# Optimization experiments

Measured on AMD Instinct MI355X. Metric: run time of the kernel, lower is better.

Reference implementation:

```python
import jax, jax.numpy as jnp
import numpy as np
import itertools

B, T, D, H, E, K = 2, 1024, 768, 3072, 8, 2


def _trigram_dirs():
    # 8 vertices of the cube {-1,+1}^3, L2-normalized rows (matches F.normalize)
    t = np.array(list(itertools.product([-1.0, 1.0], repeat=3)), dtype=np.float32)[:E]
    t = t / np.linalg.norm(t, axis=1, keepdims=True)
    return jnp.asarray(t)


def setup_inputs() -> dict:
    key = jax.random.key(0)
    k1, k2, k3, k4 = jax.random.split(key, 4)
    x = jax.random.normal(k1, (B, T, D), jnp.float32)
    Wr = jax.random.normal(k2, (3, D), jnp.float32) * 0.02
    W1 = jax.random.normal(k3, (E, D, H), jnp.float32) * 0.02
    W2 = jax.random.normal(k4, (E, H, D), jnp.float32) * 0.02
    return {"x": x, "Wr": Wr, "W1": W1, "W2": W2}


def reference(x, Wr, W1, W2):
    Bb, Tt, Dd = x.shape
    xf = x.reshape(-1, Dd)                       # (N, D)
    dirs = _trigram_dirs()                       # (E, 3)
    z3 = xf @ Wr.T                               # (N, 3)
    logits = z3 @ dirs.T                         # (N, E)
    probs = jax.nn.softmax(logits, axis=-1)
    topv, topi = jax.lax.top_k(probs, K)         # (N, K)
    topv = topv / topv.sum(axis=-1, keepdims=True)
    N = xf.shape[0]
    # dense gate matrix: gates[n, e] = sum_k topv[n,k] * [topi[n,k]==e]
    gates = jnp.zeros((N, E), xf.dtype).at[jnp.arange(N)[:, None], topi].add(topv)
    # dense-all-experts equivalent of the masked gather/scatter loop
    h = jax.nn.gelu(jnp.einsum('nd,edh->neh', xf, W1), approximate=False)
    y = jnp.einsum('neh,ehd->ned', h, W2)
    out = jnp.einsum('ne,ned->nd', gates, y).reshape(Bb, Tt, Dd)
    tokens_per_expert = probs.mean(axis=0)
    aux_loss = 0.01 * jnp.mean((tokens_per_expert - 1.0 / E) ** 2)
    return out, aux_loss
```

## Files before the change

kernel.cpp:

```cpp
#include <hip/hip_runtime.h>
#include <hip/hip_bf16.h>
#include <math.h>

#define DD 768
#define HH 3072
#define EE 8
#define NN 2048
#define PP 5120
#define PT 40

typedef __attribute__((ext_vector_type(8))) short short8;
typedef __attribute__((ext_vector_type(4))) float floatx4;

typedef const __attribute__((address_space(1))) void gas_void;
typedef __attribute__((address_space(3))) void las_void;

__device__ __forceinline__ void gld16(const void* g, void* l) {
    __builtin_amdgcn_global_load_lds((gas_void*)g, (las_void*)l, 16, 0, 0);
}

__device__ __forceinline__ unsigned short f2bf(float f) {
    union { float f; unsigned int u; } v; v.f = f;
    unsigned int u = v.u;
    u += 0x7fffu + ((u >> 16) & 1u);
    return (unsigned short)(u >> 16);
}

__global__ __launch_bounds__(256) void routing_kernel(
    const float* __restrict__ x, const float* __restrict__ Wr,
    int* __restrict__ counts, float* __restrict__ psum,
    int* __restrict__ top_e, float* __restrict__ top_g)
{
    __shared__ float wr[3 * DD];
    __shared__ float lpsum[EE];
    int tid = threadIdx.x;
    for (int i = tid; i < 3 * DD; i += 256) wr[i] = Wr[i];
    if (tid < EE) lpsum[tid] = 0.f;
    __syncthreads();

    int n = blockIdx.x * 256 + tid;
    const float4* xp = (const float4*)(x + (size_t)n * DD);
    float z0 = 0.f, z1 = 0.f, z2 = 0.f;
#pragma unroll 8
    for (int i = 0; i < DD / 4; i++) {
        float4 v = xp[i];
        int d = i * 4;
        z0 = fmaf(v.x, wr[d], z0);         z0 = fmaf(v.y, wr[d+1], z0);
        z0 = fmaf(v.z, wr[d+2], z0);       z0 = fmaf(v.w, wr[d+3], z0);
        z1 = fmaf(v.x, wr[DD+d], z1);      z1 = fmaf(v.y, wr[DD+d+1], z1);
        z1 = fmaf(v.z, wr[DD+d+2], z1);    z1 = fmaf(v.w, wr[DD+d+3], z1);
        z2 = fmaf(v.x, wr[2*DD+d], z2);    z2 = fmaf(v.y, wr[2*DD+d+1], z2);
        z2 = fmaf(v.z, wr[2*DD+d+2], z2);  z2 = fmaf(v.w, wr[2*DD+d+3], z2);
    }

    const float r3 = 0.57735026918962576f;
    float p[EE];
    float mx = -1e30f;
#pragma unroll
    for (int e = 0; e < EE; e++) {
        float s0 = (e & 4) ? z0 : -z0;
        float s1 = (e & 2) ? z1 : -z1;
        float s2 = (e & 1) ? z2 : -z2;
        p[e] = (s0 + s1 + s2) * r3;
        mx = fmaxf(mx, p[e]);
    }
    float sum = 0.f;
#pragma unroll
    for (int e = 0; e < EE; e++) { p[e] = expf(p[e] - mx); sum += p[e]; }
    float inv_s = 1.f / sum;
#pragma unroll
    for (int e = 0; e < EE; e++) p[e] *= inv_s;

    int e1 = 0; float p1 = p[0];
#pragma unroll
    for (int e = 1; e < EE; e++) if (p[e] > p1) { p1 = p[e]; e1 = e; }
    int e2 = -1; float p2 = -1.f;
#pragma unroll
    for (int e = 0; e < EE; e++) if (e != e1 && p[e] > p2) { p2 = p[e]; e2 = e; }
    float inv_t = 1.f / (p1 + p2);
    top_e[2*n]   = e1;  top_g[2*n]   = p1 * inv_t;
    top_e[2*n+1] = e2;  top_g[2*n+1] = p2 * inv_t;
    atomicAdd(&counts[e1], 1);
    atomicAdd(&counts[e2], 1);

#pragma unroll
    for (int e = 0; e < EE; e++) atomicAdd(&lpsum[e], p[e]);
    __syncthreads();
    if (tid < EE) atomicAdd(&psum[tid], lpsum[tid]);
}

__global__ void scan_aux_kernel(const int* __restrict__ counts, const float* __restrict__ psum,
                                int* __restrict__ cursor, int* __restrict__ poffs,
                                float* __restrict__ out_aux)
{
    if (threadIdx.x == 0) {
        int run = 0;
        for (int e = 0; e < EE; e++) {
            poffs[e] = run;
            cursor[e] = run;
            run += ((counts[e] + 127) >> 7) << 7;
        }
        poffs[EE] = run;
        float s = 0.f;
        for (int e = 0; e < EE; e++) {
            float t = psum[e] * (1.f / NN) - (1.f / EE);
            s += t * t;
        }
        *out_aux = 0.01f * (s * (1.f / EE));
    }
}

__global__ __launch_bounds__(256) void scatter_kernel(
    const int* __restrict__ top_e, int* __restrict__ cursor,
    int* __restrict__ row_tok, int* __restrict__ inv_row)
{
    int n = blockIdx.x * 256 + threadIdx.x;
#pragma unroll
    for (int k = 0; k < 2; k++) {
        int e = top_e[2*n + k];
        int pos = atomicAdd(&cursor[e], 1);
        row_tok[pos]    = n;
        inv_row[2*n+k]  = pos;
    }
}

__global__ __launch_bounds__(192) void gather_cast_kernel(
    const float* __restrict__ x, const int* __restrict__ counts,
    const int* __restrict__ poffs, const int* __restrict__ row_tok,
    unsigned short* __restrict__ xg)
{
    int t = threadIdx.x;
    int pr = blockIdx.x * 4 + t / 48;
    int c0 = (t % 48) * 16;
    int e = 0;
#pragma unroll
    for (int i = 0; i < EE - 1; i++) if (pr >= poffs[i + 1]) e = i + 1;
    int local = pr - poffs[e];
    unsigned short* dst = xg + (size_t)pr * DD + c0;
    if (local < counts[e]) {
        int tok = row_tok[pr];
        const float4* sp = (const float4*)(x + (size_t)tok * DD + c0);
        alignas(16) unsigned short tmp[16];
#pragma unroll
        for (int j = 0; j < 4; j++) {
            float4 v = sp[j];
            tmp[4*j+0] = f2bf(v.x); tmp[4*j+1] = f2bf(v.y);
            tmp[4*j+2] = f2bf(v.z); tmp[4*j+3] = f2bf(v.w);
        }
        *(uint4*)dst       = *(uint4*)&tmp[0];
        *(uint4*)(dst + 8) = *(uint4*)&tmp[8];
    } else {
        uint4 z = {0, 0, 0, 0};
        *(uint4*)dst       = z;
        *(uint4*)(dst + 8) = z;
    }
}

__global__ __launch_bounds__(256) void transpose_cast_kernel(
    const float* __restrict__ W1, const float* __restrict__ W2,
    unsigned short* __restrict__ w1t, unsigned short* __restrict__ w2t)
{
    int z = blockIdx.z, e = blockIdx.y, bx = blockIdx.x;
    const float* src; unsigned short* dst; int R, C, rt, ct;
    if (z == 0) { R = DD; C = HH; src = W1 + (size_t)e * R * C; dst = w1t + (size_t)e * R * C; }
    else        { R = HH; C = DD; src = W2 + (size_t)e * R * C; dst = w2t + (size_t)e * R * C; }
    rt = bx / (C / 64); ct = bx % (C / 64);
    int r0 = rt * 64, c0 = ct * 64;

    __shared__ unsigned short tile[64][66];
    int tid = threadIdx.x;
    int lr = tid >> 2, lc = (tid & 3) * 16;
    const float4* sp = (const float4*)(src + (size_t)(r0 + lr) * C + c0 + lc);
#pragma unroll
    for (int j = 0; j < 4; j++) {
        float4 v = sp[j];
        tile[lr][lc + 4*j + 0] = f2bf(v.x);
        tile[lr][lc + 4*j + 1] = f2bf(v.y);
        tile[lr][lc + 4*j + 2] = f2bf(v.z);
        tile[lr][lc + 4*j + 3] = f2bf(v.w);
    }
    __syncthreads();
    int oc = tid >> 2, orr = (tid & 3) * 16;
    alignas(16) unsigned short tmp[16];
#pragma unroll
    for (int j = 0; j < 16; j++) tmp[j] = tile[orr + j][oc];
    unsigned short* dp = dst + (size_t)(c0 + oc) * R + r0 + orr;
    *(uint4*)dp       = *(uint4*)&tmp[0];
    *(uint4*)(dp + 8) = *(uint4*)&tmp[8];
}

__global__ __launch_bounds__(256) void gemm1_kernel(
    const unsigned short* __restrict__ xg, const unsigned short* __restrict__ w1t,
    unsigned short* __restrict__ h, const int* __restrict__ poffs)
{
    int t = blockIdx.x;
    if (t * 128 >= poffs[EE]) return;
    int e = 0;
#pragma unroll
    for (int i = 0; i < EE - 1; i++) if (t * 128 >= poffs[i + 1]) e = i + 1;
    int row0 = t * 128, n0 = blockIdx.y * 128;

    __shared__ alignas(16) unsigned short As[2][128][32];
    __shared__ alignas(16) unsigned short Bs[2][128][32];

    int tid = threadIdx.x;
    int w = tid >> 6, lane = tid & 63;
    int quad = lane >> 4, l15 = lane & 15;
    int wm = (w & 1) * 64, wn = (w >> 1) * 64;

    const unsigned short* abase = xg + (size_t)row0 * DD;
    const unsigned short* bbase = w1t + (size_t)e * HH * DD + (size_t)n0 * DD;

    int c0 = w * 64 + lane, c1 = 256 + c0;
    const unsigned short* ga0 = abase + (c0 >> 2) * DD + (c0 & 3) * 8;
    const unsigned short* ga1 = abase + (c1 >> 2) * DD + (c1 & 3) * 8;
    const unsigned short* gb0 = bbase + (c0 >> 2) * DD + (c0 & 3) * 8;
    const unsigned short* gb1 = bbase + (c1 >> 2) * DD + (c1 & 3) * 8;
    int lofs0 = (w * 64) * 8;
    int lofs1 = (256 + w * 64) * 8;

    floatx4 acc[4][4];
#pragma unroll
    for (int i = 0; i < 4; i++)
#pragma unroll
        for (int j = 0; j < 4; j++)
#pragma unroll
            for (int r = 0; r < 4; r++) acc[i][j][r] = 0.f;

    const int NT = DD / 32;
    gld16(ga0, &As[0][0][0] + lofs0);
    gld16(ga1, &As[0][0][0] + lofs1);
    gld16(gb0, &Bs[0][0][0] + lofs0);
    gld16(gb1, &Bs[0][0][0] + lofs1);
    __syncthreads();

    for (int kt = 0; kt < NT; kt++) {
        int cur = kt & 1;
        if (kt + 1 < NT) {
            int k0 = (kt + 1) * 32;
            unsigned short* nA = &As[cur ^ 1][0][0];
            unsigned short* nB = &Bs[cur ^ 1][0][0];
            gld16(ga0 + k0, nA + lofs0);
            gld16(ga1 + k0, nA + lofs1);
            gld16(gb0 + k0, nB + lofs0);
            gld16(gb1 + k0, nB + lofs1);
        }
        short8 afr[4], bfr[4];
#pragma unroll
        for (int fm = 0; fm < 4; fm++) afr[fm] = *(const short8*)&As[cur][wm + fm*16 + l15][quad * 8];
#pragma unroll
        for (int fn = 0; fn < 4; fn++) bfr[fn] = *(const short8*)&Bs[cur][wn + fn*16 + l15][quad * 8];
#pragma unroll
        for (int fm = 0; fm < 4; fm++)
#pragma unroll
            for (int fn = 0; fn < 4; fn++)
                acc[fm][fn] = __builtin_amdgcn_mfma_f32_16x16x32_bf16(afr[fm], bfr[fn], acc[fm][fn], 0, 0, 0);
        __syncthreads();
    }

#pragma unroll
    for (int fm = 0; fm < 4; fm++)
#pragma unroll
        for (int r = 0; r < 4; r++) {
            int rt = wm + fm * 16 + quad * 4 + r;
            size_t hrow = (size_t)(row0 + rt) * HH;
#pragma unroll
            for (int fn = 0; fn < 4; fn++) {
                int col = n0 + wn + fn * 16 + l15;
                float v = acc[fm][fn][r];
                float g = 0.5f * v * (1.f + erff(v * 0.70710678118654752f));
                h[hrow + col] = f2bf(g);
            }
        }
}

__global__ __launch_bounds__(256) void gemm2_kernel(
    const unsigned short* __restrict__ h, const unsigned short* __restrict__ w2t,
    float* __restrict__ ybuf, const int* __restrict__ poffs)
{
    int t = blockIdx.x;
    if (t * 128 >= poffs[EE]) return;
    int e = 0;
#pragma unroll
    for (int i = 0; i < EE - 1; i++) if (t * 128 >= poffs[i + 1]) e = i + 1;
    int row0 = t * 128, n0 = blockIdx.y * 128;
    int kz = blockIdx.z;

    __shared__ alignas(16) unsigned short As[2][128][32];
    __shared__ alignas(16) unsigned short Bs[2][128][32];

    int tid = threadIdx.x;
    int w = tid >> 6, lane = tid & 63;
    int quad = lane >> 4, l15 = lane & 15;
    int wm = (w & 1) * 64, wn = (w >> 1) * 64;

    const unsigned short* abase = h + (size_t)row0 * HH + kz * (HH / 2);
    const unsigned short* bbase = w2t + (size_t)e * DD * HH + (size_t)n0 * HH + kz * (HH / 2);

    int c0 = w * 64 + lane, c1 = 256 + c0;
    const unsigned short* ga0 = abase + (c0 >> 2) * HH + (c0 & 3) * 8;
    const unsigned short* ga1 = abase + (c1 >> 2) * HH + (c1 & 3) * 8;
    const unsigned short* gb0 = bbase + (c0 >> 2) * HH + (c0 & 3) * 8;
    const unsigned short* gb1 = bbase + (c1 >> 2) * HH + (c1 & 3) * 8;
    int lofs0 = (w * 64) * 8;
    int lofs1 = (256 + w * 64) * 8;

    floatx4 acc[4][4];
#pragma unroll
    for (int i = 0; i < 4; i++)
#pragma unroll
        for (int j = 0; j < 4; j++)
#pragma unroll
            for (int r = 0; r < 4; r++) acc[i][j][r] = 0.f;

    const int NT = (HH / 2) / 32;
    gld16(ga0, &As[0][0][0] + lofs0);
    gld16(ga1, &As[0][0][0] + lofs1);
    gld16(gb0, &Bs[0][0][0] + lofs0);
    gld16(gb1, &Bs[0][0][0] + lofs1);
    __syncthreads();

    for (int kt = 0; kt < NT; kt++) {
        int cur = kt & 1;
        if (kt + 1 < NT) {
            int k0 = (kt + 1) * 32;
            unsigned short* nA = &As[cur ^ 1][0][0];
            unsigned short* nB = &Bs[cur ^ 1][0][0];
            gld16(ga0 + k0, nA + lofs0);
            gld16(ga1 + k0, nA + lofs1);
            gld16(gb0 + k0, nB + lofs0);
            gld16(gb1 + k0, nB + lofs1);
        }
        short8 afr[4], bfr[4];
#pragma unroll
        for (int fm = 0; fm < 4; fm++) afr[fm] = *(const short8*)&As[cur][wm + fm*16 + l15][quad * 8];
#pragma unroll
        for (int fn = 0; fn < 4; fn++) bfr[fn] = *(const short8*)&Bs[cur][wn + fn*16 + l15][quad * 8];
#pragma unroll
        for (int fm = 0; fm < 4; fm++)
#pragma unroll
            for (int fn = 0; fn < 4; fn++)
                acc[fm][fn] = __builtin_amdgcn_mfma_f32_16x16x32_bf16(afr[fm], bfr[fn], acc[fm][fn], 0, 0, 0);
        __syncthreads();
    }

    float* yb = ybuf + (size_t)kz * PP * DD + (size_t)row0 * DD;
#pragma unroll
    for (int fm = 0; fm < 4; fm++)
#pragma unroll
        for (int r = 0; r < 4; r++) {
            int rt = wm + fm * 16 + quad * 4 + r;
            float* op = yb + (size_t)rt * DD + n0 + wn;
#pragma unroll
            for (int fn = 0; fn < 4; fn++)
                op[fn * 16 + l15] = acc[fm][fn][r];
        }
}

__global__ __launch_bounds__(192) void combine_kernel(
    const float* __restrict__ ybuf, const int* __restrict__ inv_row,
    const float* __restrict__ top_g, float* __restrict__ out)
{
    int n = blockIdx.x;
    int c = threadIdx.x * 4;
    int r0 = inv_row[2*n], r1 = inv_row[2*n+1];
    float g0 = top_g[2*n], g1 = top_g[2*n+1];
    const size_t S = (size_t)PP * DD;
    const float* y0 = ybuf + (size_t)r0 * DD + c;
    const float* y1 = ybuf + (size_t)r1 * DD + c;
    float4 a0 = *(const float4*)y0, b0 = *(const float4*)(y0 + S);
    float4 a1 = *(const float4*)y1, b1 = *(const float4*)(y1 + S);
    float4 o;
    o.x = g0 * (a0.x + b0.x) + g1 * (a1.x + b1.x);
    o.y = g0 * (a0.y + b0.y) + g1 * (a1.y + b1.y);
    o.z = g0 * (a0.z + b0.z) + g1 * (a1.z + b1.z);
    o.w = g0 * (a0.w + b0.w) + g1 * (a1.w + b1.w);
    *(float4*)(out + (size_t)n * DD + c) = o;
}

extern "C" void kernel_launch(void* const* d_in, const int* in_sizes, int n_in,
                              void* d_out, int out_size, void* d_ws, size_t ws_size,
                              hipStream_t stream)
{
    const float* x  = (const float*)d_in[0];
    const float* Wr = (const float*)d_in[1];
    const float* W1 = (const float*)d_in[2];
    const float* W2 = (const float*)d_in[3];
    float* out = (float*)d_out;

    char* ws = (char*)d_ws;
    int*   counts   = (int*)(ws + 0);
    int*   cursor   = (int*)(ws + 32);
    float* psum     = (float*)(ws + 64);
    int*   poffs    = (int*)(ws + 96);
    int*   top_e    = (int*)(ws + 1024);
    float* top_g    = (float*)(ws + 1024 + 16384);
    int*   row_tok  = (int*)(ws + 1024 + 2 * 16384);
    int*   inv_row  = (int*)(ws + 1024 + 2 * 16384 + PP * 4);
    size_t off = (size_t)(1024 + 2 * 16384 + PP * 4 + 16384 + 255) & ~(size_t)255;
    unsigned short* xg  = (unsigned short*)(ws + off); off += (size_t)PP * DD * 2;
    unsigned short* hbf = (unsigned short*)(ws + off); off += (size_t)PP * HH * 2;
    unsigned short* w1t = (unsigned short*)(ws + off); off += (size_t)EE * DD * HH * 2;
    unsigned short* w2t = (unsigned short*)(ws + off);
    float* ybuf = (float*)w1t;

    hipMemsetAsync(ws, 0, 96, stream);

    transpose_cast_kernel<<<dim3(576, EE, 2), 256, 0, stream>>>(W1, W2, w1t, w2t);
    routing_kernel<<<dim3(NN / 256), 256, 0, stream>>>(x, Wr, counts, psum, top_e, top_g);
    scan_aux_kernel<<<1, 64, 0, stream>>>(counts, psum, cursor, poffs, out + (size_t)NN * DD);
    scatter_kernel<<<dim3(NN / 256), 256, 0, stream>>>(top_e, cursor, row_tok, inv_row);
    gather_cast_kernel<<<dim3(PP / 4), 192, 0, stream>>>(x, counts, poffs, row_tok, xg);
    gemm1_kernel<<<dim3(PT, HH / 128), 256, 0, stream>>>(xg, w1t, hbf, poffs);
    gemm2_kernel<<<dim3(PT, DD / 128, 2), 256, 0, stream>>>(hbf, w2t, ybuf, poffs);
    combine_kernel<<<dim3(NN), 192, 0, stream>>>(ybuf, inv_row, top_g, out);
}
```

Before: 383.2 us.

## Split routing dot products across 16 lanes and batch transpose tiles per block

The routing kernel now gives each token to 16 lanes that read strided float4 chunks of its row and combine partial sums with xor shuffles. The old layout had one thread per token, which left only 8 blocks and uncoalesced row-wise loads. The transpose-cast kernel now processes four 64x64 tiles per block and prefetches the next tile's loads into registers while the current tile is transposed, which cuts block count fourfold. The cost is extra shuffles and idle lanes in the routing epilogue, plus more barriers and register pressure in the transpose.

```diff
diff --git a/kernel.cpp b/kernel.cpp
--- a/kernel.cpp
+++ b/kernel.cpp
@@ -38,13 +38,14 @@
     if (tid < EE) lpsum[tid] = 0.f;
     __syncthreads();
 
-    int n = blockIdx.x * 256 + tid;
-    const float4* xp = (const float4*)(x + (size_t)n * DD);
+    int sub = tid & 15;
+    int n = blockIdx.x * 16 + (tid >> 4);
+    const float* xr = x + (size_t)n * DD;
     float z0 = 0.f, z1 = 0.f, z2 = 0.f;
-#pragma unroll 8
-    for (int i = 0; i < DD / 4; i++) {
-        float4 v = xp[i];
-        int d = i * 4;
+#pragma unroll
+    for (int i = 0; i < DD / 64; i++) {
+        int d = i * 64 + sub * 4;
+        float4 v = *(const float4*)(xr + d);
         z0 = fmaf(v.x, wr[d], z0);         z0 = fmaf(v.y, wr[d+1], z0);
         z0 = fmaf(v.z, wr[d+2], z0);       z0 = fmaf(v.w, wr[d+3], z0);
         z1 = fmaf(v.x, wr[DD+d], z1);      z1 = fmaf(v.y, wr[DD+d+1], z1);
@@ -52,39 +53,46 @@
         z2 = fmaf(v.x, wr[2*DD+d], z2);    z2 = fmaf(v.y, wr[2*DD+d+1], z2);
         z2 = fmaf(v.z, wr[2*DD+d+2], z2);  z2 = fmaf(v.w, wr[2*DD+d+3], z2);
     }
-
-    const float r3 = 0.57735026918962576f;
-    float p[EE];
-    float mx = -1e30f;
-#pragma unroll
-    for (int e = 0; e < EE; e++) {
-        float s0 = (e & 4) ? z0 : -z0;
-        float s1 = (e & 2) ? z1 : -z1;
-        float s2 = (e & 1) ? z2 : -z2;
-        p[e] = (s0 + s1 + s2) * r3;
-        mx = fmaxf(mx, p[e]);
-    }
-    float sum = 0.f;
-#pragma unroll
-    for (int e = 0; e < EE; e++) { p[e] = expf(p[e] - mx); sum += p[e]; }
-    float inv_s = 1.f / sum;
-#pragma unroll
-    for (int e = 0; e < EE; e++) p[e] *= inv_s;
-
-    int e1 = 0; float p1 = p[0];
-#pragma unroll
-    for (int e = 1; e < EE; e++) if (p[e] > p1) { p1 = p[e]; e1 = e; }
-    int e2 = -1; float p2 = -1.f;
-#pragma unroll
-    for (int e = 0; e < EE; e++) if (e != e1 && p[e] > p2) { p2 = p[e]; e2 = e; }
-    float inv_t = 1.f / (p1 + p2);
-    top_e[2*n]   = e1;  top_g[2*n]   = p1 * inv_t;
-    top_e[2*n+1] = e2;  top_g[2*n+1] = p2 * inv_t;
-    atomicAdd(&counts[e1], 1);
-    atomicAdd(&counts[e2], 1);
-
-#pragma unroll
-    for (int e = 0; e < EE; e++) atomicAdd(&lpsum[e], p[e]);
+#pragma unroll
+    for (int m = 8; m; m >>= 1) {
+        z0 += __shfl_xor(z0, m, 16);
+        z1 += __shfl_xor(z1, m, 16);
+        z2 += __shfl_xor(z2, m, 16);
+    }
+
+    if (sub == 0) {
+        const float r3 = 0.57735026918962576f;
+        float p[EE];
+        float mx = -1e30f;
+#pragma unroll
+        for (int e = 0; e < EE; e++) {
+            float s0 = (e & 4) ? z0 : -z0;
+            float s1 = (e & 2) ? z1 : -z1;
+            float s2 = (e & 1) ? z2 : -z2;
+            p[e] = (s0 + s1 + s2) * r3;
+            mx = fmaxf(mx, p[e]);
+        }
+        float sum = 0.f;
+#pragma unroll
+        for (int e = 0; e < EE; e++) { p[e] = expf(p[e] - mx); sum += p[e]; }
+        float inv_s = 1.f / sum;
+#pragma unroll
+        for (int e = 0; e < EE; e++) p[e] *= inv_s;
+
+        int e1 = 0; float p1 = p[0];
+#pragma unroll
+        for (int e = 1; e < EE; e++) if (p[e] > p1) { p1 = p[e]; e1 = e; }
+        int e2 = -1; float p2 = -1.f;
+#pragma unroll
+        for (int e = 0; e < EE; e++) if (e != e1 && p[e] > p2) { p2 = p[e]; e2 = e; }
+        float inv_t = 1.f / (p1 + p2);
+        top_e[2*n]   = e1;  top_g[2*n]   = p1 * inv_t;
+        top_e[2*n+1] = e2;  top_g[2*n+1] = p2 * inv_t;
+        atomicAdd(&counts[e1], 1);
+        atomicAdd(&counts[e2], 1);
+#pragma unroll
+        for (int e = 0; e < EE; e++) atomicAdd(&lpsum[e], p[e]);
+    }
     __syncthreads();
     if (tid < EE) atomicAdd(&psum[tid], lpsum[tid]);
 }
@@ -161,32 +169,47 @@
     unsigned short* __restrict__ w1t, unsigned short* __restrict__ w2t)
 {
     int z = blockIdx.z, e = blockIdx.y, bx = blockIdx.x;
-    const float* src; unsigned short* dst; int R, C, rt, ct;
-    if (z == 0) { R = DD; C = HH; src = W1 + (size_t)e * R * C; dst = w1t + (size_t)e * R * C; }
-    else        { R = HH; C = DD; src = W2 + (size_t)e * R * C; dst = w2t + (size_t)e * R * C; }
-    rt = bx / (C / 64); ct = bx % (C / 64);
-    int r0 = rt * 64, c0 = ct * 64;
+    const float* src; unsigned short* dst; int R, C, SC;
+    if (z == 0) { R = DD; C = HH; SC = 12; src = W1 + (size_t)e * R * C; dst = w1t + (size_t)e * R * C; }
+    else        { R = HH; C = DD; SC = 3;  src = W2 + (size_t)e * R * C; dst = w2t + (size_t)e * R * C; }
+    int rt = bx / SC, cs = bx % SC;
+    int r0 = rt * 64, cbase = cs * 256;
 
     __shared__ unsigned short tile[64][66];
     int tid = threadIdx.x;
     int lr = tid >> 2, lc = (tid & 3) * 16;
-    const float4* sp = (const float4*)(src + (size_t)(r0 + lr) * C + c0 + lc);
-#pragma unroll
-    for (int j = 0; j < 4; j++) {
-        float4 v = sp[j];
-        tile[lr][lc + 4*j + 0] = f2bf(v.x);
-        tile[lr][lc + 4*j + 1] = f2bf(v.y);
-        tile[lr][lc + 4*j + 2] = f2bf(v.z);
-        tile[lr][lc + 4*j + 3] = f2bf(v.w);
-    }
-    __syncthreads();
     int oc = tid >> 2, orr = (tid & 3) * 16;
-    alignas(16) unsigned short tmp[16];
-#pragma unroll
-    for (int j = 0; j < 16; j++) tmp[j] = tile[orr + j][oc];
-    unsigned short* dp = dst + (size_t)(c0 + oc) * R + r0 + orr;
-    *(uint4*)dp       = *(uint4*)&tmp[0];
-    *(uint4*)(dp + 8) = *(uint4*)&tmp[8];
+    const float* srow = src + (size_t)(r0 + lr) * C + lc;
+
+    float4 v0, v1, v2, v3;
+    {
+        const float4* sp = (const float4*)(srow + cbase);
+        v0 = sp[0]; v1 = sp[1]; v2 = sp[2]; v3 = sp[3];
+    }
+#pragma unroll
+    for (int i = 0; i < 4; i++) {
+        int c0 = cbase + i * 64;
+        if (i) __syncthreads();
+        tile[lr][lc+ 0]=f2bf(v0.x); tile[lr][lc+ 1]=f2bf(v0.y);
+        tile[lr][lc+ 2]=f2bf(v0.z); tile[lr][lc+ 3]=f2bf(v0.w);
+        tile[lr][lc+ 4]=f2bf(v1.x); tile[lr][lc+ 5]=f2bf(v1.y);
+        tile[lr][lc+ 6]=f2bf(v1.z); tile[lr][lc+ 7]=f2bf(v1.w);
+        tile[lr][lc+ 8]=f2bf(v2.x); tile[lr][lc+ 9]=f2bf(v2.y);
+        tile[lr][lc+10]=f2bf(v2.z); tile[lr][lc+11]=f2bf(v2.w);
+        tile[lr][lc+12]=f2bf(v3.x); tile[lr][lc+13]=f2bf(v3.y);
+        tile[lr][lc+14]=f2bf(v3.z); tile[lr][lc+15]=f2bf(v3.w);
+        if (i < 3) {
+            const float4* sp = (const float4*)(srow + c0 + 64);
+            v0 = sp[0]; v1 = sp[1]; v2 = sp[2]; v3 = sp[3];
+        }
+        __syncthreads();
+        alignas(16) unsigned short tmp[16];
+#pragma unroll
+        for (int j = 0; j < 16; j++) tmp[j] = tile[orr + j][oc];
+        unsigned short* dp = dst + (size_t)(c0 + oc) * R + r0 + orr;
+        *(uint4*)dp       = *(uint4*)&tmp[0];
+        *(uint4*)(dp + 8) = *(uint4*)&tmp[8];
+    }
 }
 
 __global__ __launch_bounds__(256) void gemm1_kernel(
@@ -406,8 +429,8 @@
 
     hipMemsetAsync(ws, 0, 96, stream);
 
-    transpose_cast_kernel<<<dim3(576, EE, 2), 256, 0, stream>>>(W1, W2, w1t, w2t);
-    routing_kernel<<<dim3(NN / 256), 256, 0, stream>>>(x, Wr, counts, psum, top_e, top_g);
+    transpose_cast_kernel<<<dim3(144, EE, 2), 256, 0, stream>>>(W1, W2, w1t, w2t);
+    routing_kernel<<<dim3(NN / 16), 256, 0, stream>>>(x, Wr, counts, psum, top_e, top_g);
     scan_aux_kernel<<<1, 64, 0, stream>>>(counts, psum, cursor, poffs, out + (size_t)NN * DD);
     scatter_kernel<<<dim3(NN / 256), 256, 0, stream>>>(top_e, cursor, row_tok, inv_row);
     gather_cast_kernel<<<dim3(PP / 4), 192, 0, stream>>>(x, counts, poffs, row_tok, xg);
```

Result: faster. 349.3 us (-8.8%).
